# Performance work log

Measured on AMD Instinct MI355X. Metric: run time of the kernel, lower is better.

## Reference

```python
import jax, jax.numpy as jnp
import numpy as np

B, V, C, P, H, D, L, F = 2, 6, 256, 200, 8, 32, 2, 1024
HW0, HW1 = (32, 88), (16, 44)
N = HW0[0] * HW0[1] + HW1[0] * HW1[1]  # 3520 keys per view
PC = (-54.0, -54.0, -5.0, 54.0, 54.0, 3.0)
GRID, OSF = (1440, 1440), 8
NEG = -1e9


def _pos_mlp(x, w1, b1, w2, b2):
    return jax.nn.relu(x @ w1.T + b1) @ w2.T + b2


def _layernorm(x, g, b):
    m = x.mean(-1, keepdims=True)
    v = ((x - m) ** 2).mean(-1, keepdims=True)
    return (x - m) * jax.lax.rsqrt(v + 1e-5) * g + b


def _mha(q, k, v, in_w, in_b, out_w, out_b, bias=None):
    c = q.shape[-1]
    dh = c // H
    wq, wk, wv = jnp.split(in_w, 3, axis=0)
    bq, bk, bv = jnp.split(in_b, 3)

    def heads(t):
        s = t.shape
        return t.reshape(s[:-1] + (H, dh)).swapaxes(-2, -3)

    qh = heads(q @ wq.T + bq)
    kh = heads(k @ wk.T + bk)
    vh = heads(v @ wv.T + bv)
    logits = jnp.einsum('...qd,...kd->...qk', qh, kh) / jnp.sqrt(jnp.asarray(dh, q.dtype))
    if bias is not None:
        logits = logits + bias
    o = jnp.einsum('...qk,...kd->...qd', jax.nn.softmax(logits, -1), vh)
    o = o.swapaxes(-2, -3).reshape(q.shape)
    return o @ out_w.T + out_b


def _forward(img_query_feat, img_query_pos, img_query_view_mask, img_feats_0, img_feats_1,
             normal_img_feats_pos_stack, lidar2img, input_hw,
             qpos_w1, qpos_b1, qpos_w2, qpos_b2, kpos_w1, kpos_b1, kpos_w2, kpos_b2,
             sa_in_w, sa_in_b, sa_out_w, sa_out_b, ca_in_w, ca_in_b, ca_out_w, ca_out_b,
             ffn_w1, ffn_b1, ffn_w2, ffn_b2, n1_g, n1_b, n2_g, n2_b, n3_g, n3_b,
             head_w1, head_b1, head_w2, head_b2):
    # flatten multi-scale image feats -> [B, V, N, C]
    keys = jnp.concatenate([img_feats_0.reshape(B, V, C, -1), img_feats_1.reshape(B, V, C, -1)], -1)
    keys = keys.transpose(0, 1, 3, 2)
    # PETR-style depth bins
    idx = jnp.arange(D, dtype=jnp.float32)
    bin_size = (PC[3] - 1.0) / (D * (1 + D))
    coords_d = jnp.maximum(1.0 + bin_size * idx * (idx + 1.0), 1e-5)
    # denormalize 2D key positions per sample
    hw = input_hw.astype(jnp.float32)
    max_xy = jnp.stack([hw[:, 1], hw[:, 0]], -1)[:, None, :]  # [B,1,2] = (w,h)
    pos2d = jax.nn.sigmoid(normal_img_feats_pos_stack) * max_xy  # [B,N,2]
    xy = jnp.broadcast_to(pos2d[:, :, None, :], (B, N, D, 2))
    xyz = jnp.concatenate([xy, jnp.ones((B, N, D, 1), xy.dtype)], -1) * coords_d[None, None, :, None]
    homo = jnp.concatenate([xyz, jnp.ones((B, N, D, 1), xy.dtype)], -1)  # [B,N,D,4]
    inv = jnp.linalg.inv(lidar2img)  # [B,V,4,4]
    cam = jnp.einsum('bndj,bvij->bvndi', homo, inv)[..., :3].reshape(B, V, N, D * 3)  # [B,V,N,96]
    # ragged view assignment -> masked attention / masked scatter-average
    mask = (img_query_view_mask > 0).transpose(0, 2, 1)  # [B,V,P]
    valid = mask.sum(-1) > 1  # views with >1 query are processed
    active = mask & valid[:, :, None]  # [B,V,P]
    sa_bias = jnp.where(active[:, :, None, None, :], 0.0, NEG)  # [B,V,1,1,P]
    q_feat = img_query_feat  # [B,C,P]
    q_pos = img_query_pos  # [B,P,3]
    centers, heights = [], []
    pos_bev = None
    for l in range(L):
        pe_q = _pos_mlp(q_pos, qpos_w1[l], qpos_b1[l], qpos_w2[l], qpos_b2[l])  # [B,P,C]
        pe_k = _pos_mlp(cam, kpos_w1[l], kpos_b1[l], kpos_w2[l], kpos_b2[l])  # [B,V,N,C]
        x = jnp.broadcast_to(q_feat.transpose(0, 2, 1)[:, None], (B, V, P, C))
        peq = jnp.broadcast_to(pe_q[:, None], (B, V, P, C))
        qkv = x + peq
        x = _layernorm(x + _mha(qkv, qkv, qkv, sa_in_w[l], sa_in_b[l], sa_out_w[l], sa_out_b[l], sa_bias), n1_g[l], n1_b[l])
        kv = keys + pe_k
        x = _layernorm(x + _mha(x + peq, kv, kv, ca_in_w[l], ca_in_b[l], ca_out_w[l], ca_out_b[l]), n2_g[l], n2_b[l])
        x = _layernorm(x + (jax.nn.relu(x @ ffn_w1[l].T + ffn_b1[l]) @ ffn_w2[l].T + ffn_b2[l]), n3_g[l], n3_b[l])
        # scatter-accumulate over views with count-based averaging
        contrib = jnp.where(active[..., None], x, 0.0)  # [B,V,P,C]
        cnt = active.sum(1).astype(x.dtype)  # [B,P]
        q_feat = (contrib.sum(1) / (cnt[..., None] + 1e-4)).transpose(0, 2, 1)  # [B,C,P]
        # prediction head (conv1d-relu-conv1d) producing center_view [B,3,P]
        h1 = jax.nn.relu(jnp.einsum('oc,bcp->bop', head_w1, q_feat) + head_b1[None, :, None])
        center = jnp.einsum('oc,bcp->bop', head_w2, h1) + head_b2[None, :, None]
        center = center + q_pos.transpose(0, 2, 1)
        q_pos = jax.lax.stop_gradient(center).transpose(0, 2, 1)
        height = center[:, 2:3]
        cx = (center[:, 0] - PC[0]) / (PC[3] - PC[0]) * (GRID[0] // OSF)
        cy = (center[:, 1] - PC[1]) / (PC[4] - PC[1]) * (GRID[1] // OSF)
        cbev = jnp.stack([cx, cy], 1)  # [B,2,P]
        centers.append(cbev)
        heights.append(height)
        pos_bev = jax.lax.stop_gradient(cbev).transpose(0, 2, 1)
    return (q_feat, q_pos, pos_bev, jnp.stack(centers), jnp.stack(heights))


def setup_inputs():
    key = jax.random.key(0)
    it = iter(jax.random.split(key, 48))

    def rn(shape, s=1.0):
        return jax.random.normal(next(it), shape, dtype=jnp.float32) * s

    inp = {}
    inp['img_query_feat'] = rn((B, C, P))
    inp['img_query_pos'] = rn((B, P, 3))
    inp['img_query_view_mask'] = jax.random.randint(next(it), (B, P, V), 0, 2, dtype=jnp.int32)
    inp['img_feats_0'] = rn((B, V, C) + HW0)
    inp['img_feats_1'] = rn((B, V, C) + HW1)
    inp['normal_img_feats_pos_stack'] = rn((1, N, 2))
    inp['lidar2img'] = jnp.broadcast_to(jnp.eye(4, dtype=jnp.float32), (B, V, 4, 4)) + 0.1 * rn((B, V, 4, 4))
    inp['input_hw'] = jnp.array([[320, 800]] * B, dtype=jnp.int32)
    s = 0.02
    inp['qpos_w1'] = rn((L, C, 3), s); inp['qpos_b1'] = jnp.zeros((L, C), jnp.float32)
    inp['qpos_w2'] = rn((L, C, C), s); inp['qpos_b2'] = jnp.zeros((L, C), jnp.float32)
    inp['kpos_w1'] = rn((L, C, D * 3), s); inp['kpos_b1'] = jnp.zeros((L, C), jnp.float32)
    inp['kpos_w2'] = rn((L, C, C), s); inp['kpos_b2'] = jnp.zeros((L, C), jnp.float32)
    inp['sa_in_w'] = rn((L, 3 * C, C), s); inp['sa_in_b'] = jnp.zeros((L, 3 * C), jnp.float32)
    inp['sa_out_w'] = rn((L, C, C), s); inp['sa_out_b'] = jnp.zeros((L, C), jnp.float32)
    inp['ca_in_w'] = rn((L, 3 * C, C), s); inp['ca_in_b'] = jnp.zeros((L, 3 * C), jnp.float32)
    inp['ca_out_w'] = rn((L, C, C), s); inp['ca_out_b'] = jnp.zeros((L, C), jnp.float32)
    inp['ffn_w1'] = rn((L, F, C), s); inp['ffn_b1'] = jnp.zeros((L, F), jnp.float32)
    inp['ffn_w2'] = rn((L, C, F), s); inp['ffn_b2'] = jnp.zeros((L, C), jnp.float32)
    for nm in ('n1', 'n2', 'n3'):
        inp[nm + '_g'] = jnp.ones((L, C), jnp.float32)
        inp[nm + '_b'] = jnp.zeros((L, C), jnp.float32)
    inp['head_w1'] = rn((C, C), s); inp['head_b1'] = jnp.zeros((C,), jnp.float32)
    inp['head_w2'] = rn((3, C), s); inp['head_b2'] = jnp.zeros((3,), jnp.float32)
    return inp


def reference(img_query_feat, img_query_pos, img_query_view_mask, img_feats_0, img_feats_1,
              normal_img_feats_pos_stack, lidar2img, input_hw,
              qpos_w1, qpos_b1, qpos_w2, qpos_b2, kpos_w1, kpos_b1, kpos_w2, kpos_b2,
              sa_in_w, sa_in_b, sa_out_w, sa_out_b, ca_in_w, ca_in_b, ca_out_w, ca_out_b,
              ffn_w1, ffn_b1, ffn_w2, ffn_b2, n1_g, n1_b, n2_g, n2_b, n3_g, n3_b,
              head_w1, head_b1, head_w2, head_b2):
    return _forward(img_query_feat, img_query_pos, img_query_view_mask, img_feats_0, img_feats_1,
                    normal_img_feats_pos_stack, lidar2img, input_hw,
                    qpos_w1, qpos_b1, qpos_w2, qpos_b2, kpos_w1, kpos_b1, kpos_w2, kpos_b2,
                    sa_in_w, sa_in_b, sa_out_w, sa_out_b, ca_in_w, ca_in_b, ca_out_w, ca_out_b,
                    ffn_w1, ffn_b1, ffn_w2, ffn_b2, n1_g, n1_b, n2_g, n2_b, n3_g, n3_b,
                    head_w1, head_b1, head_w2, head_b2)
```

## Files before the change

kernel.cpp:

```cpp
#include <hip/hip_runtime.h>
#include <math.h>

#define B_ 2
#define V_ 6
#define C_ 256
#define P_ 200
#define H_ 8
#define D_ 32
#define L_ 2
#define F_ 1024
#define N_ 3520
#define HW0T 2816
#define HW1T 704
#define BV_ (B_*V_)
#define NKTOT (BV_*N_)
#define ROWS_ (BV_*P_)
#define BVH_ (BV_*H_)
#define NEGV -1000000000.0f

static const size_t O_KEYS = 0;
static const size_t O_CAM  = O_KEYS + (size_t)NKTOT*C_;
static const size_t O_PEK  = O_CAM  + (size_t)NKTOT*96;
static const size_t O_BIG  = O_PEK  + (size_t)NKTOT*C_;
static const size_t O_HID  = O_BIG;
static const size_t O_KVP  = O_BIG;
static const size_t O_PEQH = O_BIG + (size_t)NKTOT*512;
static const size_t O_PEQ  = O_PEQH + 102400;
static const size_t O_X    = O_PEQ  + 102400;
static const size_t O_QKV  = O_X    + 614400;
static const size_t O_SAIN = O_QKV  + 614400;
static const size_t O_ATT  = O_SAIN + 1843200;
static const size_t O_QPROJ= O_ATT  + 614400;
static const size_t O_PROJ = O_QPROJ+ 614400;
static const size_t O_TMP  = O_PROJ + 614400;
static const size_t O_FFNH = O_TMP  + 614400;
static const size_t O_QF   = O_FFNH + 2457600;
static const size_t O_H1   = O_QF   + 102400;
static const size_t O_QPOS = O_H1   + 102400;
static const size_t O_ACTF = O_QPOS + 1200;
static const size_t O_ACTN = O_ACTF + 2400;
static const size_t O_INV  = O_ACTN + 2400;
static const size_t O_PML  = O_INV  + 192;
static const size_t O_PACC = O_PML  + 307200;

#define OO_QFEAT   0
#define OO_QPOS    102400
#define OO_POSBEV  103600
#define OO_CENTERS 104400
#define OO_HEIGHTS 106000

__global__ void inv4_kernel(const float* __restrict__ A, float* __restrict__ Ainv) {
    int t = blockIdx.x * blockDim.x + threadIdx.x;
    if (t >= BV_) return;
    const float* m = A + t*16;
    float i0  =  m[5]*m[10]*m[15] - m[5]*m[11]*m[14] - m[9]*m[6]*m[15] + m[9]*m[7]*m[14] + m[13]*m[6]*m[11] - m[13]*m[7]*m[10];
    float i4  = -m[4]*m[10]*m[15] + m[4]*m[11]*m[14] + m[8]*m[6]*m[15] - m[8]*m[7]*m[14] - m[12]*m[6]*m[11] + m[12]*m[7]*m[10];
    float i8  =  m[4]*m[9]*m[15]  - m[4]*m[11]*m[13] - m[8]*m[5]*m[15] + m[8]*m[7]*m[13] + m[12]*m[5]*m[11] - m[12]*m[7]*m[9];
    float i12 = -m[4]*m[9]*m[14]  + m[4]*m[10]*m[13] + m[8]*m[5]*m[14] - m[8]*m[6]*m[13] - m[12]*m[5]*m[10] + m[12]*m[6]*m[9];
    float i1  = -m[1]*m[10]*m[15] + m[1]*m[11]*m[14] + m[9]*m[2]*m[15] - m[9]*m[3]*m[14] - m[13]*m[2]*m[11] + m[13]*m[3]*m[10];
    float i5  =  m[0]*m[10]*m[15] - m[0]*m[11]*m[14] - m[8]*m[2]*m[15] + m[8]*m[3]*m[14] + m[12]*m[2]*m[11] - m[12]*m[3]*m[10];
    float i9  = -m[0]*m[9]*m[15]  + m[0]*m[11]*m[13] + m[8]*m[1]*m[15] - m[8]*m[3]*m[13] - m[12]*m[1]*m[11] + m[12]*m[3]*m[9];
    float i13 =  m[0]*m[9]*m[14]  - m[0]*m[10]*m[13] - m[8]*m[1]*m[14] + m[8]*m[2]*m[13] + m[12]*m[1]*m[10] - m[12]*m[2]*m[9];
    float i2  =  m[1]*m[6]*m[15]  - m[1]*m[7]*m[14]  - m[5]*m[2]*m[15] + m[5]*m[3]*m[14] + m[13]*m[2]*m[7]  - m[13]*m[3]*m[6];
    float i6  = -m[0]*m[6]*m[15]  + m[0]*m[7]*m[14]  + m[4]*m[2]*m[15] - m[4]*m[3]*m[14] - m[12]*m[2]*m[7]  + m[12]*m[3]*m[6];
    float i10 =  m[0]*m[5]*m[15]  - m[0]*m[7]*m[13]  - m[4]*m[1]*m[15] + m[4]*m[3]*m[13] + m[12]*m[1]*m[7]  - m[12]*m[3]*m[5];
    float i14 = -m[0]*m[5]*m[14]  + m[0]*m[6]*m[13]  + m[4]*m[1]*m[14] - m[4]*m[2]*m[13] - m[12]*m[1]*m[6]  + m[12]*m[2]*m[5];
    float i3  = -m[1]*m[6]*m[11]  + m[1]*m[7]*m[10]  + m[5]*m[2]*m[11] - m[5]*m[3]*m[10] - m[9]*m[2]*m[7]   + m[9]*m[3]*m[6];
    float i7  =  m[0]*m[6]*m[11]  - m[0]*m[7]*m[10]  - m[4]*m[2]*m[11] + m[4]*m[3]*m[10] + m[8]*m[2]*m[7]   - m[8]*m[3]*m[6];
    float i11 = -m[0]*m[5]*m[11]  + m[0]*m[7]*m[9]   + m[4]*m[1]*m[11] - m[4]*m[3]*m[9]  - m[8]*m[1]*m[7]   + m[8]*m[3]*m[5];
    float i15 =  m[0]*m[5]*m[10]  - m[0]*m[6]*m[9]   - m[4]*m[1]*m[10] + m[4]*m[2]*m[9]  + m[8]*m[1]*m[6]   - m[8]*m[2]*m[5];
    float det = m[0]*i0 + m[1]*i4 + m[2]*i8 + m[3]*i12;
    float r = 1.0f / det;
    float* o = Ainv + t*16;
    o[0]=i0*r;  o[1]=i1*r;  o[2]=i2*r;  o[3]=i3*r;
    o[4]=i4*r;  o[5]=i5*r;  o[6]=i6*r;  o[7]=i7*r;
    o[8]=i8*r;  o[9]=i9*r;  o[10]=i10*r;o[11]=i11*r;
    o[12]=i12*r;o[13]=i13*r;o[14]=i14*r;o[15]=i15*r;
}

__global__ void cam_kernel(const float* __restrict__ pos, const int* __restrict__ hw,
                           const float* __restrict__ inv, float* __restrict__ cam) {
    int g = blockIdx.x * blockDim.x + threadIdx.x;
    const int total = BV_ * N_ * D_;
    if (g >= total) return;
    int d  = g & 31;
    int n  = (g >> 5) % N_;
    int bv = g / (N_ * D_);
    int b  = bv / V_;
    float sx = pos[n*2+0], sy = pos[n*2+1];
    float mx = (float)hw[b*2+1], my = (float)hw[b*2+0];
    float px = mx / (1.0f + expf(-sx));
    float py = my / (1.0f + expf(-sy));
    const float binsz = 53.0f / 1056.0f;
    float cd = fmaxf(1.0f + binsz * (float)d * (float)(d+1), 1e-5f);
    float h0 = px*cd, h1 = py*cd, h2 = cd, h3 = 1.0f;
    const float* iv = inv + bv*16;
    float* o = cam + ((size_t)bv * N_ + n) * 96 + d*3;
    o[0] = iv[0]*h0 + iv[1]*h1 + iv[2]*h2  + iv[3]*h3;
    o[1] = iv[4]*h0 + iv[5]*h1 + iv[6]*h2  + iv[7]*h3;
    o[2] = iv[8]*h0 + iv[9]*h1 + iv[10]*h2 + iv[11]*h3;
}

__global__ void transpose_keys_kernel(const float* __restrict__ src, float* __restrict__ keys,
                                      int HW, int n_off) {
    __shared__ float tile[32][33];
    int bv = blockIdx.z;
    int x0 = blockIdx.x * 32;
    int c0 = blockIdx.y * 32;
    int tx = threadIdx.x, ty = threadIdx.y;
    tile[ty][tx] = src[((size_t)bv * C_ + c0 + ty) * HW + x0 + tx];
    __syncthreads();
    keys[((size_t)bv * N_ + n_off + x0 + ty) * C_ + c0 + tx] = tile[tx][ty];
}

__global__ void mask_kernel(const int* __restrict__ qvm, float* __restrict__ actF, float* __restrict__ actNeg) {
    int bv = blockIdx.x;
    int b = bv / V_, v = bv % V_;
    int p = threadIdx.x;
    int m = 0;
    if (p < P_) m = (qvm[(b*P_ + p)*V_ + v] > 0) ? 1 : 0;
    __shared__ int s[256];
    s[threadIdx.x] = m;
    __syncthreads();
    for (int off = 128; off > 0; off >>= 1) {
        if (threadIdx.x < off) s[threadIdx.x] += s[threadIdx.x + off];
        __syncthreads();
    }
    int valid = (s[0] > 1);
    if (p < P_) {
        int act = m && valid;
        actF[bv*P_ + p]   = act ? 1.0f : 0.0f;
        actNeg[bv*P_ + p] = act ? 0.0f : NEGV;
    }
}

template<int RELU, int FUSE>
__global__ __launch_bounds__(256) void gemm_kernel(
    const float* __restrict__ A, const float* __restrict__ A2,
    const float* __restrict__ W, const float* __restrict__ bias,
    float* __restrict__ Cmat, int M, int N, int K)
{
    __shared__ float As[16][68];
    __shared__ float Ws[16][68];
    int m0 = blockIdx.y * 64, n0 = blockIdx.x * 64;
    int tid = threadIdx.x;
    int tx = tid & 15, ty = tid >> 4;
    int ar = tid >> 2;
    int ac = (tid & 3) * 4;
    float acc[4][4] = {};
    for (int k0 = 0; k0 < K; k0 += 16) {
        #pragma unroll
        for (int j = 0; j < 4; ++j) {
            int kk = ac + j;
            int m = m0 + ar;
            float v = 0.0f;
            if (m < M && (k0 + kk) < K) {
                v = A[(size_t)m * K + k0 + kk];
                if (FUSE) v += A2[(size_t)m * K + k0 + kk];
            }
            As[kk][ar] = v;
        }
        #pragma unroll
        for (int j = 0; j < 4; ++j) {
            int kk = ac + j;
            int n = n0 + ar;
            float v = 0.0f;
            if (n < N && (k0 + kk) < K) v = W[(size_t)n * K + k0 + kk];
            Ws[kk][ar] = v;
        }
        __syncthreads();
        #pragma unroll
        for (int kk = 0; kk < 16; ++kk) {
            const float4 a = *(const float4*)&As[kk][ty*4];
            const float4 w = *(const float4*)&Ws[kk][tx*4];
            acc[0][0] = fmaf(a.x, w.x, acc[0][0]); acc[0][1] = fmaf(a.x, w.y, acc[0][1]);
            acc[0][2] = fmaf(a.x, w.z, acc[0][2]); acc[0][3] = fmaf(a.x, w.w, acc[0][3]);
            acc[1][0] = fmaf(a.y, w.x, acc[1][0]); acc[1][1] = fmaf(a.y, w.y, acc[1][1]);
            acc[1][2] = fmaf(a.y, w.z, acc[1][2]); acc[1][3] = fmaf(a.y, w.w, acc[1][3]);
            acc[2][0] = fmaf(a.z, w.x, acc[2][0]); acc[2][1] = fmaf(a.z, w.y, acc[2][1]);
            acc[2][2] = fmaf(a.z, w.z, acc[2][2]); acc[2][3] = fmaf(a.z, w.w, acc[2][3]);
            acc[3][0] = fmaf(a.w, w.x, acc[3][0]); acc[3][1] = fmaf(a.w, w.y, acc[3][1]);
            acc[3][2] = fmaf(a.w, w.z, acc[3][2]); acc[3][3] = fmaf(a.w, w.w, acc[3][3]);
        }
        __syncthreads();
    }
    #pragma unroll
    for (int i = 0; i < 4; ++i) {
        int m = m0 + ty*4 + i;
        if (m >= M) continue;
        #pragma unroll
        for (int j = 0; j < 4; ++j) {
            int n = n0 + tx*4 + j;
            if (n >= N) continue;
            float v = acc[i][j] + bias[n];
            if (RELU) v = fmaxf(v, 0.0f);
            Cmat[(size_t)m * N + n] = v;
        }
    }
}

template<int RELU, int FUSE>
__global__ __launch_bounds__(256) void gemm128_kernel(
    const float* __restrict__ A, const float* __restrict__ A2,
    const float* __restrict__ W, const float* __restrict__ bias,
    float* __restrict__ Cmat, int M, int N, int K)
{
    __shared__ float As[16][132];
    __shared__ float Ws[16][132];
    const int tid = threadIdx.x;
    const int m0 = blockIdx.x * 128;
    const int n0 = blockIdx.y * 128;
    const int tx = tid & 15, ty = tid >> 4;

    const int srow = tid >> 2;
    const int skc  = (tid & 3) * 4;

    const int arow0 = min(m0 + srow,      M - 1);
    const int arow1 = min(m0 + srow + 64, M - 1);
    const float* Ab0 = A + (size_t)arow0 * K + skc;
    const float* Ab1 = A + (size_t)arow1 * K + skc;
    const float* A2b0 = FUSE ? (A2 + (size_t)arow0 * K + skc) : nullptr;
    const float* A2b1 = FUSE ? (A2 + (size_t)arow1 * K + skc) : nullptr;
    const float* Wb0 = W + (size_t)(n0 + srow) * K + skc;
    const float* Wb1 = W + (size_t)(n0 + srow + 64) * K + skc;

    float acc[8][8] = {};

    for (int k0 = 0; k0 < K; k0 += 16) {
        float4 a0 = *(const float4*)(Ab0 + k0);
        float4 a1 = *(const float4*)(Ab1 + k0);
        float4 w0 = *(const float4*)(Wb0 + k0);
        float4 w1 = *(const float4*)(Wb1 + k0);
        if (FUSE) {
            float4 e0 = *(const float4*)(A2b0 + k0);
            float4 e1 = *(const float4*)(A2b1 + k0);
            a0.x += e0.x; a0.y += e0.y; a0.z += e0.z; a0.w += e0.w;
            a1.x += e1.x; a1.y += e1.y; a1.z += e1.z; a1.w += e1.w;
        }
        __syncthreads();
        As[skc+0][srow] = a0.x; As[skc+1][srow] = a0.y; As[skc+2][srow] = a0.z; As[skc+3][srow] = a0.w;
        As[skc+0][srow+64] = a1.x; As[skc+1][srow+64] = a1.y; As[skc+2][srow+64] = a1.z; As[skc+3][srow+64] = a1.w;
        Ws[skc+0][srow] = w0.x; Ws[skc+1][srow] = w0.y; Ws[skc+2][srow] = w0.z; Ws[skc+3][srow] = w0.w;
        Ws[skc+0][srow+64] = w1.x; Ws[skc+1][srow+64] = w1.y; Ws[skc+2][srow+64] = w1.z; Ws[skc+3][srow+64] = w1.w;
        __syncthreads();
        #pragma unroll
        for (int kk = 0; kk < 16; ++kk) {
            float av[8], bv[8];
            *(float4*)&av[0] = *(const float4*)&As[kk][ty*8];
            *(float4*)&av[4] = *(const float4*)&As[kk][ty*8+4];
            *(float4*)&bv[0] = *(const float4*)&Ws[kk][tx*8];
            *(float4*)&bv[4] = *(const float4*)&Ws[kk][tx*8+4];
            #pragma unroll
            for (int i = 0; i < 8; ++i)
                #pragma unroll
                for (int j = 0; j < 8; ++j)
                    acc[i][j] = fmaf(av[i], bv[j], acc[i][j]);
        }
    }

    float bn[8];
    #pragma unroll
    for (int j = 0; j < 8; ++j) bn[j] = bias[n0 + tx*8 + j];

    #pragma unroll
    for (int i = 0; i < 8; ++i) {
        int m = m0 + ty*8 + i;
        if (m >= M) continue;
        float o[8];
        #pragma unroll
        for (int j = 0; j < 8; ++j) {
            float v = acc[i][j] + bn[j];
            if (RELU) v = fmaxf(v, 0.0f);
            o[j] = v;
        }
        float* cp = Cmat + (size_t)m * N + n0 + tx*8;
        *(float4*)cp       = *(float4*)&o[0];
        *(float4*)(cp + 4) = *(float4*)&o[4];
    }
}

__global__ __launch_bounds__(256) void ln_kernel(const float* __restrict__ Xa, const float* __restrict__ Xb,
    const float* __restrict__ g, const float* __restrict__ beta, float* __restrict__ out, int rows)
{
    int wid  = (blockIdx.x * blockDim.x + threadIdx.x) >> 6;
    int lane = threadIdx.x & 63;
    if (wid >= rows) return;
    float4 x = ((const float4*)(Xa + (size_t)wid * C_))[lane];
    float4 y = ((const float4*)(Xb + (size_t)wid * C_))[lane];
    x.x += y.x; x.y += y.y; x.z += y.z; x.w += y.w;
    float s = x.x + x.y + x.z + x.w;
    for (int d = 32; d > 0; d >>= 1) s += __shfl_xor(s, d);
    float mean = s * (1.0f / C_);
    float dx = x.x - mean, dy = x.y - mean, dz = x.z - mean, dw = x.w - mean;
    float v = dx*dx + dy*dy + dz*dz + dw*dw;
    for (int d = 32; d > 0; d >>= 1) v += __shfl_xor(v, d);
    float rstd = 1.0f / sqrtf(v * (1.0f / C_) + 1e-5f);
    float4 gg = ((const float4*)g)[lane];
    float4 bb = ((const float4*)beta)[lane];
    float4 o;
    o.x = dx * rstd * gg.x + bb.x;
    o.y = dy * rstd * gg.y + bb.y;
    o.z = dz * rstd * gg.z + bb.z;
    o.w = dw * rstd * gg.w + bb.w;
    ((float4*)(out + (size_t)wid * C_))[lane] = o;
}

__global__ void xbcast_kernel(const float* __restrict__ qf, float* __restrict__ x) {
    __shared__ float tile[32][33];
    int b  = blockIdx.z;
    int p0 = blockIdx.x * 32, c0 = blockIdx.y * 32;
    int tx = threadIdx.x, ty = threadIdx.y;
    float v = 0.0f;
    if (p0 + tx < P_) v = qf[((size_t)b * C_ + c0 + ty) * P_ + p0 + tx];
    tile[ty][tx] = v;
    __syncthreads();
    int p = p0 + ty;
    if (p < P_) {
        float val = tile[tx][ty];
        #pragma unroll
        for (int vv = 0; vv < V_; ++vv)
            x[(((size_t)(b*V_ + vv) * P_) + p) * C_ + c0 + tx] = val;
    }
}

__global__ void bcast_add_kernel(const float* __restrict__ x, const float* __restrict__ peq, float* __restrict__ out) {
    int g = blockIdx.x * blockDim.x + threadIdx.x;
    const int total = ROWS_ * C_ / 4;
    if (g >= total) return;
    int c4 = g & 63;
    int rest = g >> 6;
    int p  = rest % P_;
    int bv = rest / P_;
    int b  = bv / V_;
    float4 xv = ((const float4*)x)[g];
    float4 pv = ((const float4*)peq)[((size_t)(b*P_ + p)) * 64 + c4];
    float4 o; o.x = xv.x + pv.x; o.y = xv.y + pv.y; o.z = xv.z + pv.z; o.w = xv.w + pv.w;
    ((float4*)out)[g] = o;
}

__global__ __launch_bounds__(256) void attn_kernel(
    const float* __restrict__ Q, int qstride,
    const float* __restrict__ Kp, int kstride,
    const float* __restrict__ Vp, int vstride,
    const float* __restrict__ biasNeg,
    float* __restrict__ pAcc, float* __restrict__ pML,
    int NK, int S, float scale)
{
    int split = blockIdx.x, bvh = blockIdx.y;
    int bv = bvh >> 3, h = bvh & 7;
    int p = threadIdx.x;
    bool act = p < P_;
    int per = (NK + S - 1) / S;
    int k0 = split * per;
    int k1 = min(NK, k0 + per);

    __shared__ float Ks[32][36];
    __shared__ float Vs[32][36];
    __shared__ float Bs[32];

    float q[32];
    const float* qrow = Q + ((size_t)bv * P_ + (act ? p : 0)) * qstride + h * 32;
    #pragma unroll
    for (int j = 0; j < 32; j += 4) {
        float4 t = *(const float4*)(qrow + j);
        q[j] = t.x; q[j+1] = t.y; q[j+2] = t.z; q[j+3] = t.w;
    }
    float m = -INFINITY, l = 0.0f;
    float acc[32] = {};

    for (int kt = k0; kt < k1; kt += 32) {
        int kmax = min(32, k1 - kt);
        __syncthreads();
        {
            int t = threadIdx.x;
            int key = t >> 3, f = (t & 7) << 2;
            if (key < kmax) {
                const float* kr = Kp + ((size_t)bv * NK + kt + key) * kstride + h*32 + f;
                *(float4*)&Ks[key][f] = *(const float4*)kr;
                const float* vr = Vp + ((size_t)bv * NK + kt + key) * vstride + h*32 + f;
                *(float4*)&Vs[key][f] = *(const float4*)vr;
            }
            if (t < kmax) Bs[t] = biasNeg ? biasNeg[bv * P_ + kt + t] : 0.0f;
        }
        __syncthreads();
        if (act) {
            for (int k = 0; k < kmax; ++k) {
                const float4* k4 = (const float4*)&Ks[k][0];
                float s0 = 0, s1 = 0, s2 = 0, s3 = 0;
                #pragma unroll
                for (int jj = 0; jj < 8; ++jj) {
                    float4 kv = k4[jj];
                    s0 = fmaf(q[4*jj+0], kv.x, s0);
                    s1 = fmaf(q[4*jj+1], kv.y, s1);
                    s2 = fmaf(q[4*jj+2], kv.z, s2);
                    s3 = fmaf(q[4*jj+3], kv.w, s3);
                }
                float s = ((s0 + s1) + (s2 + s3)) * scale + Bs[k];
                const float4* v4 = (const float4*)&Vs[k][0];
                if (__any(s > m)) {
                    float mn = fmaxf(m, s);
                    float corr = __expf(m - mn);
                    float pr = __expf(s - mn);
                    m = mn;
                    l = fmaf(l, corr, pr);
                    #pragma unroll
                    for (int jj = 0; jj < 8; ++jj) {
                        float4 vv = v4[jj];
                        acc[4*jj+0] = fmaf(acc[4*jj+0], corr, pr * vv.x);
                        acc[4*jj+1] = fmaf(acc[4*jj+1], corr, pr * vv.y);
                        acc[4*jj+2] = fmaf(acc[4*jj+2], corr, pr * vv.z);
                        acc[4*jj+3] = fmaf(acc[4*jj+3], corr, pr * vv.w);
                    }
                } else {
                    float pr = __expf(s - m);
                    l += pr;
                    #pragma unroll
                    for (int jj = 0; jj < 8; ++jj) {
                        float4 vv = v4[jj];
                        acc[4*jj+0] = fmaf(pr, vv.x, acc[4*jj+0]);
                        acc[4*jj+1] = fmaf(pr, vv.y, acc[4*jj+1]);
                        acc[4*jj+2] = fmaf(pr, vv.z, acc[4*jj+2]);
                        acc[4*jj+3] = fmaf(pr, vv.w, acc[4*jj+3]);
                    }
                }
            }
        }
    }
    if (act) {
        size_t base = ((size_t)bvh * S + split) * 32 * P_ + p;
        #pragma unroll
        for (int j = 0; j < 32; ++j) pAcc[base + (size_t)j * P_] = acc[j];
        size_t mb = ((size_t)bvh * S + split) * 2 * P_ + p;
        pML[mb] = m; pML[mb + P_] = l;
    }
}

template<int S>
__global__ void attn_combine_kernel(const float* __restrict__ pAcc, const float* __restrict__ pML,
                                    float* __restrict__ Out)
{
    int g = blockIdx.x * blockDim.x + threadIdx.x;
    if (g >= BVH_ * P_) return;
    int p = g % P_;
    int bvh = g / P_;
    int bv = bvh >> 3, h = bvh & 7;
    float mg = -INFINITY;
    #pragma unroll
    for (int s = 0; s < S; ++s) mg = fmaxf(mg, pML[((size_t)bvh * S + s) * 2 * P_ + p]);
    float w[S];
    float L = 0.0f;
    #pragma unroll
    for (int s = 0; s < S; ++s) {
        float ms = pML[((size_t)bvh * S + s) * 2 * P_ + p];
        float ls = pML[((size_t)bvh * S + s) * 2 * P_ + P_ + p];
        float ws = __expf(ms - mg);
        w[s] = ws;
        L = fmaf(ls, ws, L);
    }
    float invL = 1.0f / L;
    float* orow = Out + ((size_t)bv * P_ + p) * C_ + h * 32;
    #pragma unroll
    for (int j = 0; j < 32; ++j) {
        float acc = 0.0f;
        #pragma unroll
        for (int s = 0; s < S; ++s)
            acc = fmaf(pAcc[(((size_t)bvh * S + s) * 32 + j) * P_ + p], w[s], acc);
        orow[j] = acc * invL;
    }
}

__global__ void agg_kernel(const float* __restrict__ x, const float* __restrict__ actF,
                           float* __restrict__ qf, float* __restrict__ qf_out) {
    int bp = blockIdx.x;
    int b = bp / P_, p = bp % P_;
    int c = threadIdx.x;
    float sum = 0.0f, cnt = 0.0f;
    #pragma unroll
    for (int v = 0; v < V_; ++v) {
        float a = actF[(b*V_ + v) * P_ + p];
        cnt += a;
        sum = fmaf(a, x[(((size_t)(b*V_ + v)) * P_ + p) * C_ + c], sum);
    }
    float r = sum / (cnt + 1e-4f);
    qf[((size_t)b * C_ + c) * P_ + p] = r;
    if (qf_out) qf_out[((size_t)b * C_ + c) * P_ + p] = r;
}

__global__ void head1_kernel(const float* __restrict__ w1, const float* __restrict__ b1,
                             const float* __restrict__ qf, float* __restrict__ h1out) {
    int g = blockIdx.x * blockDim.x + threadIdx.x;
    if (g >= B_ * C_ * P_) return;
    int p = g % P_;
    int o = (g / P_) % C_;
    int b = g / (P_ * C_);
    float s = b1[o];
    const float* wr = w1 + (size_t)o * C_;
    const float* qc = qf + (size_t)b * C_ * P_ + p;
    for (int c = 0; c < C_; ++c) s = fmaf(wr[c], qc[(size_t)c * P_], s);
    h1out[g] = fmaxf(s, 0.0f);
}

__global__ void center_kernel(const float* __restrict__ w2, const float* __restrict__ b2,
                              const float* __restrict__ h1, const float* __restrict__ qpos_in,
                              float* __restrict__ qpos_ws, float* __restrict__ out, int layer) {
    int g = blockIdx.x * blockDim.x + threadIdx.x;
    if (g >= B_ * P_) return;
    int p = g % P_, b = g / P_;
    float c0 = b2[0], c1 = b2[1], c2 = b2[2];
    const float* hc = h1 + (size_t)b * C_ * P_ + p;
    for (int c = 0; c < C_; ++c) {
        float hv = hc[(size_t)c * P_];
        c0 = fmaf(w2[c], hv, c0);
        c1 = fmaf(w2[C_ + c], hv, c1);
        c2 = fmaf(w2[2*C_ + c], hv, c2);
    }
    const float* qp = qpos_in + ((size_t)b * P_ + p) * 3;
    c0 += qp[0]; c1 += qp[1]; c2 += qp[2];
    float* qw = qpos_ws + ((size_t)b * P_ + p) * 3;
    qw[0] = c0; qw[1] = c1; qw[2] = c2;
    float cx = (c0 + 54.0f) / 108.0f * 180.0f;
    float cy = (c1 + 54.0f) / 108.0f * 180.0f;
    float* centers = out + OO_CENTERS + ((size_t)(layer * B_ + b) * 2) * P_;
    centers[p] = cx;
    centers[P_ + p] = cy;
    out[OO_HEIGHTS + (size_t)(layer * B_ + b) * P_ + p] = c2;
    if (layer == L_ - 1) {
        float* qo = out + OO_QPOS + ((size_t)b * P_ + p) * 3;
        qo[0] = c0; qo[1] = c1; qo[2] = c2;
        float* pb = out + OO_POSBEV + ((size_t)b * P_ + p) * 2;
        pb[0] = cx; pb[1] = cy;
    }
}

extern "C" void kernel_launch(void* const* d_in, const int* in_sizes, int n_in,
                              void* d_out, int out_size, void* d_ws, size_t ws_size,
                              hipStream_t stream) {
    const float* in_qfeat = (const float*)d_in[0];
    const float* in_qpos  = (const float*)d_in[1];
    const int*   in_qvm   = (const int*)d_in[2];
    const float* in_f0    = (const float*)d_in[3];
    const float* in_f1    = (const float*)d_in[4];
    const float* in_pos   = (const float*)d_in[5];
    const float* in_l2i   = (const float*)d_in[6];
    const int*   in_hw    = (const int*)d_in[7];
    const float* qpos_w1  = (const float*)d_in[8];
    const float* qpos_b1  = (const float*)d_in[9];
    const float* qpos_w2  = (const float*)d_in[10];
    const float* qpos_b2  = (const float*)d_in[11];
    const float* kpos_w1  = (const float*)d_in[12];
    const float* kpos_b1  = (const float*)d_in[13];
    const float* kpos_w2  = (const float*)d_in[14];
    const float* kpos_b2  = (const float*)d_in[15];
    const float* sa_in_w  = (const float*)d_in[16];
    const float* sa_in_b  = (const float*)d_in[17];
    const float* sa_out_w = (const float*)d_in[18];
    const float* sa_out_b = (const float*)d_in[19];
    const float* ca_in_w  = (const float*)d_in[20];
    const float* ca_in_b  = (const float*)d_in[21];
    const float* ca_out_w = (const float*)d_in[22];
    const float* ca_out_b = (const float*)d_in[23];
    const float* ffn_w1   = (const float*)d_in[24];
    const float* ffn_b1   = (const float*)d_in[25];
    const float* ffn_w2   = (const float*)d_in[26];
    const float* ffn_b2   = (const float*)d_in[27];
    const float* n1_g     = (const float*)d_in[28];
    const float* n1_b     = (const float*)d_in[29];
    const float* n2_g     = (const float*)d_in[30];
    const float* n2_b     = (const float*)d_in[31];
    const float* n3_g     = (const float*)d_in[32];
    const float* n3_b     = (const float*)d_in[33];
    const float* head_w1  = (const float*)d_in[34];
    const float* head_b1  = (const float*)d_in[35];
    const float* head_w2  = (const float*)d_in[36];
    const float* head_b2  = (const float*)d_in[37];

    float* ws   = (float*)d_ws;
    float* KEYS = ws + O_KEYS;
    float* CAM  = ws + O_CAM;
    float* PEK  = ws + O_PEK;
    float* HID  = ws + O_HID;
    float* KVP  = ws + O_KVP;
    float* PEQH = ws + O_PEQH;
    float* PEQ  = ws + O_PEQ;
    float* X    = ws + O_X;
    float* QKV  = ws + O_QKV;
    float* SAIN = ws + O_SAIN;
    float* ATT  = ws + O_ATT;
    float* QPROJ= ws + O_QPROJ;
    float* PROJ = ws + O_PROJ;
    float* TMP  = ws + O_TMP;
    float* FFNH = ws + O_FFNH;
    float* QF   = ws + O_QF;
    float* H1   = ws + O_H1;
    float* QPOS = ws + O_QPOS;
    float* ACTF = ws + O_ACTF;
    float* ACTN = ws + O_ACTN;
    float* INV  = ws + O_INV;
    float* PML  = ws + O_PML;
    float* PACC = ws + O_PACC;
    float* OUT  = (float*)d_out;

    const float scale = 0.17677669529663687f;

    inv4_kernel<<<1, 64, 0, stream>>>(in_l2i, INV);
    cam_kernel<<<(BV_*N_*D_ + 255)/256, 256, 0, stream>>>(in_pos, in_hw, INV, CAM);
    transpose_keys_kernel<<<dim3(HW0T/32, C_/32, BV_), dim3(32,32), 0, stream>>>(in_f0, KEYS, HW0T, 0);
    transpose_keys_kernel<<<dim3(HW1T/32, C_/32, BV_), dim3(32,32), 0, stream>>>(in_f1, KEYS, HW1T, HW0T);
    mask_kernel<<<BV_, 256, 0, stream>>>(in_qvm, ACTF, ACTN);

    const int MT_NK = NKTOT / 128;
    const int MT_R  = (ROWS_ + 127) / 128;

    for (int l = 0; l < L_; ++l) {
        const float* qf_src   = (l == 0) ? in_qfeat : QF;
        const float* qpos_src = (l == 0) ? in_qpos  : QPOS;

        gemm_kernel<1,0><<<dim3(4,7), 256, 0, stream>>>(qpos_src, nullptr, qpos_w1 + l*C_*3, qpos_b1 + l*C_, PEQH, 400, C_, 3);
        gemm_kernel<0,0><<<dim3(4,7), 256, 0, stream>>>(PEQH, nullptr, qpos_w2 + l*C_*C_, qpos_b2 + l*C_, PEQ, 400, C_, C_);

        gemm128_kernel<1,0><<<dim3(MT_NK, 2), 256, 0, stream>>>(CAM, nullptr, kpos_w1 + l*C_*96, kpos_b1 + l*C_, HID, NKTOT, C_, 96);
        gemm128_kernel<0,0><<<dim3(MT_NK, 2), 256, 0, stream>>>(HID, nullptr, kpos_w2 + l*C_*C_, kpos_b2 + l*C_, PEK, NKTOT, C_, C_);

        xbcast_kernel<<<dim3(7, 8, B_), dim3(32,32), 0, stream>>>(qf_src, X);
        bcast_add_kernel<<<600, 256, 0, stream>>>(X, PEQ, QKV);

        gemm128_kernel<0,0><<<dim3(MT_R, 6), 256, 0, stream>>>(QKV, nullptr, sa_in_w + l*768*C_, sa_in_b + l*768, SAIN, ROWS_, 768, C_);
        attn_kernel<<<dim3(4, BVH_), 256, 0, stream>>>(SAIN, 768, SAIN + 256, 768, SAIN + 512, 768, ACTN, PACC, PML, P_, 4, scale);
        attn_combine_kernel<4><<<(BVH_*P_)/256, 256, 0, stream>>>(PACC, PML, ATT);
        gemm128_kernel<0,0><<<dim3(MT_R, 2), 256, 0, stream>>>(ATT, nullptr, sa_out_w + l*C_*C_, sa_out_b + l*C_, PROJ, ROWS_, C_, C_);
        ln_kernel<<<600, 256, 0, stream>>>(X, PROJ, n1_g + l*C_, n1_b + l*C_, X, ROWS_);

        bcast_add_kernel<<<600, 256, 0, stream>>>(X, PEQ, TMP);
        gemm128_kernel<0,0><<<dim3(MT_R, 2), 256, 0, stream>>>(TMP, nullptr, ca_in_w + l*768*C_, ca_in_b + l*768, QPROJ, ROWS_, C_, C_);
        gemm128_kernel<0,1><<<dim3(MT_NK, 4), 256, 0, stream>>>(KEYS, PEK, ca_in_w + l*768*C_ + C_*C_, ca_in_b + l*768 + C_, KVP, NKTOT, 512, C_);
        attn_kernel<<<dim3(8, BVH_), 256, 0, stream>>>(QPROJ, 256, KVP, 512, KVP + 256, 512, nullptr, PACC, PML, N_, 8, scale);
        attn_combine_kernel<8><<<(BVH_*P_)/256, 256, 0, stream>>>(PACC, PML, ATT);
        gemm128_kernel<0,0><<<dim3(MT_R, 2), 256, 0, stream>>>(ATT, nullptr, ca_out_w + l*C_*C_, ca_out_b + l*C_, PROJ, ROWS_, C_, C_);
        ln_kernel<<<600, 256, 0, stream>>>(X, PROJ, n2_g + l*C_, n2_b + l*C_, X, ROWS_);

        gemm128_kernel<1,0><<<dim3(MT_R, 8), 256, 0, stream>>>(X, nullptr, ffn_w1 + l*F_*C_, ffn_b1 + l*F_, FFNH, ROWS_, F_, C_);
        gemm128_kernel<0,0><<<dim3(MT_R, 2), 256, 0, stream>>>(FFNH, nullptr, ffn_w2 + l*C_*F_, ffn_b2 + l*C_, PROJ, ROWS_, C_, F_);
        ln_kernel<<<600, 256, 0, stream>>>(X, PROJ, n3_g + l*C_, n3_b + l*C_, X, ROWS_);

        agg_kernel<<<B_*P_, 256, 0, stream>>>(X, ACTF, QF, (l == L_-1) ? (OUT + OO_QFEAT) : nullptr);

        head1_kernel<<<(B_*C_*P_ + 255)/256, 256, 0, stream>>>(head_w1, head_b1, QF, H1);
        center_kernel<<<(B_*P_ + 255)/256, 256, 0, stream>>>(head_w2, head_b2, H1, qpos_src, QPOS, OUT, l);
    }
}
```

Baseline: 2.054 ms.

## Add 64-row GEMM for small matmuls, block-wise softmax in attention, fused head kernel

Introduces a 64x128-tile GEMM and uses it for all the 2400-row query-side projections and FFN, so more blocks fill the GPU. Self-attention moves from 4 to 8 key splits. The attention inner loop now computes all 32 scores per tile, then does one max and rescale per tile instead of a per-key branchy online softmax, padding with zero keys and -inf bias. The head MLP and center kernels are fused into one per-query kernel that reads a transposed copy of the query features written by agg_kernel. The costs are more register pressure from the 32-score array and one extra write in agg_kernel.

```diff
diff --git a/kernel.cpp b/kernel.cpp
--- a/kernel.cpp
+++ b/kernel.cpp
@@ -35,8 +35,8 @@
 static const size_t O_TMP  = O_PROJ + 614400;
 static const size_t O_FFNH = O_TMP  + 614400;
 static const size_t O_QF   = O_FFNH + 2457600;
-static const size_t O_H1   = O_QF   + 102400;
-static const size_t O_QPOS = O_H1   + 102400;
+static const size_t O_QFT  = O_QF   + 102400;
+static const size_t O_QPOS = O_QFT  + 102400;
 static const size_t O_ACTF = O_QPOS + 1200;
 static const size_t O_ACTN = O_ACTF + 2400;
 static const size_t O_INV  = O_ACTN + 2400;
@@ -211,7 +211,6 @@
     const int m0 = blockIdx.x * 128;
     const int n0 = blockIdx.y * 128;
     const int tx = tid & 15, ty = tid >> 4;
-
     const int srow = tid >> 2;
     const int skc  = (tid & 3) * 4;
 
@@ -265,6 +264,74 @@
     #pragma unroll
     for (int i = 0; i < 8; ++i) {
         int m = m0 + ty*8 + i;
+        if (m >= M) continue;
+        float o[8];
+        #pragma unroll
+        for (int j = 0; j < 8; ++j) {
+            float v = acc[i][j] + bn[j];
+            if (RELU) v = fmaxf(v, 0.0f);
+            o[j] = v;
+        }
+        float* cp = Cmat + (size_t)m * N + n0 + tx*8;
+        *(float4*)cp       = *(float4*)&o[0];
+        *(float4*)(cp + 4) = *(float4*)&o[4];
+    }
+}
+
+template<int RELU>
+__global__ __launch_bounds__(256) void gemm64_kernel(
+    const float* __restrict__ A,
+    const float* __restrict__ W, const float* __restrict__ bias,
+    float* __restrict__ Cmat, int M, int N, int K)
+{
+    __shared__ float As[16][68];
+    __shared__ float Ws[16][132];
+    const int tid = threadIdx.x;
+    const int m0 = blockIdx.x * 64;
+    const int n0 = blockIdx.y * 128;
+    const int tx = tid & 15, ty = tid >> 4;
+
+    const int ar  = tid >> 2;
+    const int kca = (tid & 3) * 4;
+    const int wr  = tid >> 1;
+    const int kcw = (tid & 1) * 8;
+
+    const int arow = min(m0 + ar, M - 1);
+    const float* Ab = A + (size_t)arow * K + kca;
+    const float* Wb = W + (size_t)(n0 + wr) * K + kcw;
+
+    float acc[4][8] = {};
+
+    for (int k0 = 0; k0 < K; k0 += 16) {
+        float4 a0 = *(const float4*)(Ab + k0);
+        float4 w0 = *(const float4*)(Wb + k0);
+        float4 w1 = *(const float4*)(Wb + k0 + 4);
+        __syncthreads();
+        As[kca+0][ar] = a0.x; As[kca+1][ar] = a0.y; As[kca+2][ar] = a0.z; As[kca+3][ar] = a0.w;
+        Ws[kcw+0][wr] = w0.x; Ws[kcw+1][wr] = w0.y; Ws[kcw+2][wr] = w0.z; Ws[kcw+3][wr] = w0.w;
+        Ws[kcw+4][wr] = w1.x; Ws[kcw+5][wr] = w1.y; Ws[kcw+6][wr] = w1.z; Ws[kcw+7][wr] = w1.w;
+        __syncthreads();
+        #pragma unroll
+        for (int kk = 0; kk < 16; ++kk) {
+            float av[4], bv[8];
+            *(float4*)&av[0] = *(const float4*)&As[kk][ty*4];
+            *(float4*)&bv[0] = *(const float4*)&Ws[kk][tx*8];
+            *(float4*)&bv[4] = *(const float4*)&Ws[kk][tx*8+4];
+            #pragma unroll
+            for (int i = 0; i < 4; ++i)
+                #pragma unroll
+                for (int j = 0; j < 8; ++j)
+                    acc[i][j] = fmaf(av[i], bv[j], acc[i][j]);
+        }
+    }
+
+    float bn[8];
+    #pragma unroll
+    for (int j = 0; j < 8; ++j) bn[j] = bias[n0 + tx*8 + j];
+
+    #pragma unroll
+    for (int i = 0; i < 4; ++i) {
+        int m = m0 + ty*4 + i;
         if (m >= M) continue;
         float o[8];
         #pragma unroll
@@ -379,12 +446,18 @@
                 *(float4*)&Ks[key][f] = *(const float4*)kr;
                 const float* vr = Vp + ((size_t)bv * NK + kt + key) * vstride + h*32 + f;
                 *(float4*)&Vs[key][f] = *(const float4*)vr;
+            } else {
+                float4 z = make_float4(0.f, 0.f, 0.f, 0.f);
+                *(float4*)&Ks[key][f] = z;
+                *(float4*)&Vs[key][f] = z;
             }
-            if (t < kmax) Bs[t] = biasNeg ? biasNeg[bv * P_ + kt + t] : 0.0f;
+            if (t < 32) Bs[t] = (t < kmax) ? (biasNeg ? biasNeg[bv * P_ + kt + t] : 0.0f) : -INFINITY;
         }
         __syncthreads();
         if (act) {
-            for (int k = 0; k < kmax; ++k) {
+            float sc[32];
+            #pragma unroll
+            for (int k = 0; k < 32; ++k) {
                 const float4* k4 = (const float4*)&Ks[k][0];
                 float s0 = 0, s1 = 0, s2 = 0, s3 = 0;
                 #pragma unroll
@@ -395,33 +468,29 @@
                     s2 = fmaf(q[4*jj+2], kv.z, s2);
                     s3 = fmaf(q[4*jj+3], kv.w, s3);
                 }
-                float s = ((s0 + s1) + (s2 + s3)) * scale + Bs[k];
+                sc[k] = ((s0 + s1) + (s2 + s3)) * scale + Bs[k];
+            }
+            float tm = sc[0];
+            #pragma unroll
+            for (int k = 1; k < 32; ++k) tm = fmaxf(tm, sc[k]);
+            float nm = fmaxf(m, tm);
+            float corr = __expf(m - nm);
+            m = nm;
+            l *= corr;
+            #pragma unroll
+            for (int j = 0; j < 32; ++j) acc[j] *= corr;
+            #pragma unroll
+            for (int k = 0; k < 32; ++k) {
+                float pr = __expf(sc[k] - nm);
+                l += pr;
                 const float4* v4 = (const float4*)&Vs[k][0];
-                if (__any(s > m)) {
-                    float mn = fmaxf(m, s);
-                    float corr = __expf(m - mn);
-                    float pr = __expf(s - mn);
-                    m = mn;
-                    l = fmaf(l, corr, pr);
-                    #pragma unroll
-                    for (int jj = 0; jj < 8; ++jj) {
-                        float4 vv = v4[jj];
-                        acc[4*jj+0] = fmaf(acc[4*jj+0], corr, pr * vv.x);
-                        acc[4*jj+1] = fmaf(acc[4*jj+1], corr, pr * vv.y);
-                        acc[4*jj+2] = fmaf(acc[4*jj+2], corr, pr * vv.z);
-                        acc[4*jj+3] = fmaf(acc[4*jj+3], corr, pr * vv.w);
-                    }
-                } else {
-                    float pr = __expf(s - m);
-                    l += pr;
-                    #pragma unroll
-                    for (int jj = 0; jj < 8; ++jj) {
-                        float4 vv = v4[jj];
-                        acc[4*jj+0] = fmaf(pr, vv.x, acc[4*jj+0]);
-                        acc[4*jj+1] = fmaf(pr, vv.y, acc[4*jj+1]);
-                        acc[4*jj+2] = fmaf(pr, vv.z, acc[4*jj+2]);
-                        acc[4*jj+3] = fmaf(pr, vv.w, acc[4*jj+3]);
-                    }
+                #pragma unroll
+                for (int jj = 0; jj < 8; ++jj) {
+                    float4 vv = v4[jj];
+                    acc[4*jj+0] = fmaf(pr, vv.x, acc[4*jj+0]);
+                    acc[4*jj+1] = fmaf(pr, vv.y, acc[4*jj+1]);
+                    acc[4*jj+2] = fmaf(pr, vv.z, acc[4*jj+2]);
+                    acc[4*jj+3] = fmaf(pr, vv.w, acc[4*jj+3]);
                 }
             }
         }
@@ -470,7 +539,7 @@
 }
 
 __global__ void agg_kernel(const float* __restrict__ x, const float* __restrict__ actF,
-                           float* __restrict__ qf, float* __restrict__ qf_out) {
+                           float* __restrict__ qf, float* __restrict__ qft, float* __restrict__ qf_out) {
     int bp = blockIdx.x;
     int b = bp / P_, p = bp % P_;
     int c = threadIdx.x;
@@ -483,52 +552,53 @@
     }
     float r = sum / (cnt + 1e-4f);
     qf[((size_t)b * C_ + c) * P_ + p] = r;
+    qft[((size_t)b * P_ + p) * C_ + c] = r;
     if (qf_out) qf_out[((size_t)b * C_ + c) * P_ + p] = r;
 }
 
-__global__ void head1_kernel(const float* __restrict__ w1, const float* __restrict__ b1,
-                             const float* __restrict__ qf, float* __restrict__ h1out) {
-    int g = blockIdx.x * blockDim.x + threadIdx.x;
-    if (g >= B_ * C_ * P_) return;
-    int p = g % P_;
-    int o = (g / P_) % C_;
-    int b = g / (P_ * C_);
-    float s = b1[o];
-    const float* wr = w1 + (size_t)o * C_;
-    const float* qc = qf + (size_t)b * C_ * P_ + p;
-    for (int c = 0; c < C_; ++c) s = fmaf(wr[c], qc[(size_t)c * P_], s);
-    h1out[g] = fmaxf(s, 0.0f);
-}
-
-__global__ void center_kernel(const float* __restrict__ w2, const float* __restrict__ b2,
-                              const float* __restrict__ h1, const float* __restrict__ qpos_in,
-                              float* __restrict__ qpos_ws, float* __restrict__ out, int layer) {
-    int g = blockIdx.x * blockDim.x + threadIdx.x;
-    if (g >= B_ * P_) return;
-    int p = g % P_, b = g / P_;
-    float c0 = b2[0], c1 = b2[1], c2 = b2[2];
-    const float* hc = h1 + (size_t)b * C_ * P_ + p;
-    for (int c = 0; c < C_; ++c) {
-        float hv = hc[(size_t)c * P_];
-        c0 = fmaf(w2[c], hv, c0);
-        c1 = fmaf(w2[C_ + c], hv, c1);
-        c2 = fmaf(w2[2*C_ + c], hv, c2);
-    }
-    const float* qp = qpos_in + ((size_t)b * P_ + p) * 3;
-    c0 += qp[0]; c1 += qp[1]; c2 += qp[2];
-    float* qw = qpos_ws + ((size_t)b * P_ + p) * 3;
-    qw[0] = c0; qw[1] = c1; qw[2] = c2;
-    float cx = (c0 + 54.0f) / 108.0f * 180.0f;
-    float cy = (c1 + 54.0f) / 108.0f * 180.0f;
-    float* centers = out + OO_CENTERS + ((size_t)(layer * B_ + b) * 2) * P_;
-    centers[p] = cx;
-    centers[P_ + p] = cy;
-    out[OO_HEIGHTS + (size_t)(layer * B_ + b) * P_ + p] = c2;
-    if (layer == L_ - 1) {
-        float* qo = out + OO_QPOS + ((size_t)b * P_ + p) * 3;
-        qo[0] = c0; qo[1] = c1; qo[2] = c2;
-        float* pb = out + OO_POSBEV + ((size_t)b * P_ + p) * 2;
-        pb[0] = cx; pb[1] = cy;
+__global__ __launch_bounds__(256) void head_kernel(
+    const float* __restrict__ w1, const float* __restrict__ b1,
+    const float* __restrict__ w2, const float* __restrict__ b2,
+    const float* __restrict__ qft, const float* __restrict__ qpos_in,
+    float* __restrict__ qpos_ws, float* __restrict__ out, int layer)
+{
+    int bp = blockIdx.x;
+    int b = bp / P_, p = bp % P_;
+    int tid = threadIdx.x;
+    __shared__ float qcol[C_];
+    __shared__ float h1s[C_];
+    qcol[tid] = qft[((size_t)b * P_ + p) * C_ + tid];
+    __syncthreads();
+    float s = b1[tid];
+    const float* wr = w1 + (size_t)tid * C_;
+    #pragma unroll 8
+    for (int c = 0; c < C_; ++c) s = fmaf(wr[c], qcol[c], s);
+    h1s[tid] = fmaxf(s, 0.0f);
+    __syncthreads();
+    int grp = tid >> 6, lane = tid & 63;
+    if (grp < 3) {
+        float part = 0.0f;
+        #pragma unroll
+        for (int c = 0; c < 4; ++c)
+            part = fmaf(w2[grp * C_ + lane + c*64], h1s[lane + c*64], part);
+        for (int d = 32; d > 0; d >>= 1) part += __shfl_xor(part, d);
+        if (lane == 0) {
+            float val = part + b2[grp] + qpos_in[((size_t)b * P_ + p) * 3 + grp];
+            qpos_ws[((size_t)b * P_ + p) * 3 + grp] = val;
+            if (grp == 2) {
+                out[OO_HEIGHTS + (size_t)(layer * B_ + b) * P_ + p] = val;
+                if (layer == L_ - 1)
+                    out[OO_QPOS + ((size_t)b * P_ + p) * 3 + 2] = val;
+            } else {
+                float cbev = (val + 54.0f) / 108.0f * 180.0f;
+                float* centers = out + OO_CENTERS + ((size_t)(layer * B_ + b) * 2) * P_;
+                centers[grp * P_ + p] = cbev;
+                if (layer == L_ - 1) {
+                    out[OO_QPOS + ((size_t)b * P_ + p) * 3 + grp] = val;
+                    out[OO_POSBEV + ((size_t)b * P_ + p) * 2 + grp] = cbev;
+                }
+            }
+        }
     }
 }
 
@@ -591,7 +661,7 @@
     float* TMP  = ws + O_TMP;
     float* FFNH = ws + O_FFNH;
     float* QF   = ws + O_QF;
-    float* H1   = ws + O_H1;
+    float* QFT  = ws + O_QFT;
     float* QPOS = ws + O_QPOS;
     float* ACTF = ws + O_ACTF;
     float* ACTN = ws + O_ACTN;
@@ -608,8 +678,8 @@
     transpose_keys_kernel<<<dim3(HW1T/32, C_/32, BV_), dim3(32,32), 0, stream>>>(in_f1, KEYS, HW1T, HW0T);
     mask_kernel<<<BV_, 256, 0, stream>>>(in_qvm, ACTF, ACTN);
 
-    const int MT_NK = NKTOT / 128;
-    const int MT_R  = (ROWS_ + 127) / 128;
+    const int MT_NK  = NKTOT / 128;
+    const int MT64_R = (ROWS_ + 63) / 64;
 
     for (int l = 0; l < L_; ++l) {
         const float* qf_src   = (l == 0) ? in_qfeat : QF;
@@ -624,27 +694,27 @@
         xbcast_kernel<<<dim3(7, 8, B_), dim3(32,32), 0, stream>>>(qf_src, X);
         bcast_add_kernel<<<600, 256, 0, stream>>>(X, PEQ, QKV);
 
-        gemm128_kernel<0,0><<<dim3(MT_R, 6), 256, 0, stream>>>(QKV, nullptr, sa_in_w + l*768*C_, sa_in_b + l*768, SAIN, ROWS_, 768, C_);
-        attn_kernel<<<dim3(4, BVH_), 256, 0, stream>>>(SAIN, 768, SAIN + 256, 768, SAIN + 512, 768, ACTN, PACC, PML, P_, 4, scale);
-        attn_combine_kernel<4><<<(BVH_*P_)/256, 256, 0, stream>>>(PACC, PML, ATT);
-        gemm128_kernel<0,0><<<dim3(MT_R, 2), 256, 0, stream>>>(ATT, nullptr, sa_out_w + l*C_*C_, sa_out_b + l*C_, PROJ, ROWS_, C_, C_);
+        gemm64_kernel<0><<<dim3(MT64_R, 6), 256, 0, stream>>>(QKV, sa_in_w + l*768*C_, sa_in_b + l*768, SAIN, ROWS_, 768, C_);
+        attn_kernel<<<dim3(8, BVH_), 256, 0, stream>>>(SAIN, 768, SAIN + 256, 768, SAIN + 512, 768, ACTN, PACC, PML, P_, 8, scale);
+        attn_combine_kernel<8><<<(BVH_*P_)/256, 256, 0, stream>>>(PACC, PML, ATT);
+        gemm64_kernel<0><<<dim3(MT64_R, 2), 256, 0, stream>>>(ATT, sa_out_w + l*C_*C_, sa_out_b + l*C_, PROJ, ROWS_, C_, C_);
         ln_kernel<<<600, 256, 0, stream>>>(X, PROJ, n1_g + l*C_, n1_b + l*C_, X, ROWS_);
 
         bcast_add_kernel<<<600, 256, 0, stream>>>(X, PEQ, TMP);
-        gemm128_kernel<0,0><<<dim3(MT_R, 2), 256, 0, stream>>>(TMP, nullptr, ca_in_w + l*768*C_, ca_in_b + l*768, QPROJ, ROWS_, C_, C_);
+        gemm64_kernel<0><<<dim3(MT64_R, 2), 256, 0, stream>>>(TMP, ca_in_w + l*768*C_, ca_in_b + l*768, QPROJ, ROWS_, C_, C_);
         gemm128_kernel<0,1><<<dim3(MT_NK, 4), 256, 0, stream>>>(KEYS, PEK, ca_in_w + l*768*C_ + C_*C_, ca_in_b + l*768 + C_, KVP, NKTOT, 512, C_);
         attn_kernel<<<dim3(8, BVH_), 256, 0, stream>>>(QPROJ, 256, KVP, 512, KVP + 256, 512, nullptr, PACC, PML, N_, 8, scale);
         attn_combine_kernel<8><<<(BVH_*P_)/256, 256, 0, stream>>>(PACC, PML, ATT);
-        gemm128_kernel<0,0><<<dim3(MT_R, 2), 256, 0, stream>>>(ATT, nullptr, ca_out_w + l*C_*C_, ca_out_b + l*C_, PROJ, ROWS_, C_, C_);
+        gemm64_kernel<0><<<dim3(MT64_R, 2), 256, 0, stream>>>(ATT, ca_out_w + l*C_*C_, ca_out_b + l*C_, PROJ, ROWS_, C_, C_);
         ln_kernel<<<600, 256, 0, stream>>>(X, PROJ, n2_g + l*C_, n2_b + l*C_, X, ROWS_);
 
-        gemm128_kernel<1,0><<<dim3(MT_R, 8), 256, 0, stream>>>(X, nullptr, ffn_w1 + l*F_*C_, ffn_b1 + l*F_, FFNH, ROWS_, F_, C_);
-        gemm128_kernel<0,0><<<dim3(MT_R, 2), 256, 0, stream>>>(FFNH, nullptr, ffn_w2 + l*C_*F_, ffn_b2 + l*C_, PROJ, ROWS_, C_, F_);
+        gemm64_kernel<1><<<dim3(MT64_R, 8), 256, 0, stream>>>(X, ffn_w1 + l*F_*C_, ffn_b1 + l*F_, FFNH, ROWS_, F_, C_);
+        gemm64_kernel<0><<<dim3(MT64_R, 2), 256, 0, stream>>>(FFNH, ffn_w2 + l*C_*F_, ffn_b2 + l*C_, PROJ, ROWS_, C_, F_);
         ln_kernel<<<600, 256, 0, stream>>>(X, PROJ, n3_g + l*C_, n3_b + l*C_, X, ROWS_);
 
-        agg_kernel<<<B_*P_, 256, 0, stream>>>(X, ACTF, QF, (l == L_-1) ? (OUT + OO_QFEAT) : nullptr);
-
-        head1_kernel<<<(B_*C_*P_ + 255)/256, 256, 0, stream>>>(head_w1, head_b1, QF, H1);
-        center_kernel<<<(B_*P_ + 255)/256, 256, 0, stream>>>(head_w2, head_b2, H1, qpos_src, QPOS, OUT, l);
-    }
-}
+        agg_kernel<<<B_*P_, 256, 0, stream>>>(X, ACTF, QF, QFT, (l == L_-1) ? (OUT + OO_QFEAT) : nullptr);
+
+        head_kernel<<<B_*P_, 256, 0, stream>>>(head_w1, head_b1, head_w2, head_b2,
+                                               QFT, qpos_src, QPOS, OUT, l);
+    }
+}
```

Result: faster. 1.931 ms (-6.0%).
